# Optimization experiments

Hardware: AMD Instinct MI355X
Metric: run time of the kernel (lower is better)

The kernel has to match this reference:

```python
import jax, jax.numpy as jnp
import numpy as np

B, S, D, H, F, M = 2, 2048, 1024, 16, 4096, 1024
HD = D // H
LR, MOM_DECAY, WD, THRESH = 0.01, 0.9, 0.01, 0.1


def rmsnorm(x, w, eps=1e-8):
    n = jnp.linalg.norm(x, axis=-1, keepdims=True) * (x.shape[-1] ** -0.5)
    return w * x / (n + eps)


def rope_sin_cos(seq_len, dim):
    inv_freq = 1.0 / (10000.0 ** (jnp.arange(0, dim, 2, dtype=jnp.float32) / dim))
    ang = jnp.arange(seq_len, dtype=jnp.float32)[:, None] * inv_freq[None, :]  # [S, dim/2]
    return jnp.sin(ang), jnp.cos(ang)


def apply_rope(x, sin, cos):
    # x: [B,H,S,hd]; sin/cos: [S,hd/2] broadcast. Matches torch source:
    # split even/odd lanes, then CONCATENATE halves (not interleave).
    x1, x2 = x[..., ::2], x[..., 1::2]
    return jnp.concatenate([x1 * cos - x2 * sin, x1 * sin + x2 * cos], axis=-1)


def lmm_mlp(z, w0, b0, w1, b1):
    return jnp.maximum(z @ w0 + b0, 0.0) @ w1 + b1


def setup_inputs() -> dict:
    key = jax.random.key(0)
    k = jax.random.split(key, 20)
    sc = 0.02
    r = lambda i, shape: jax.random.normal(k[i], shape, jnp.float32) * sc
    return {
        'x': jax.random.normal(k[0], (B, S, D), jnp.float32),
        'mask': jnp.tril(jnp.ones((1, 1, S, S), dtype=bool)),
        'wq': r(1, (D, D)), 'wk': r(2, (D, D)), 'wv': r(3, (D, D)), 'wo': r(4, (D, D)),
        'n1': jnp.ones(D, jnp.float32), 'n2': jnp.ones(D, jnp.float32), 'n3': jnp.ones(D, jnp.float32),
        'ffn_w1': r(5, (D, F)), 'ffn_w2': r(6, (D, F)), 'ffn_w3': r(7, (F, D)),
        'pk_w': r(8, (D, M)), 'pk_b': jnp.zeros(M, jnp.float32),
        'pv_w': r(9, (D, M)), 'pv_b': jnp.zeros(M, jnp.float32),
        'pq_w': r(10, (D, M)), 'pq_b': jnp.zeros(M, jnp.float32),
        'l0_w': r(11, (M, M)), 'l0_b': jnp.zeros(M, jnp.float32),
        'l1_w': r(12, (M, M)), 'l1_b': jnp.zeros(M, jnp.float32),
        'm0_w': jnp.zeros((M, M), jnp.float32), 'm0_b': jnp.zeros(M, jnp.float32),
        'm1_w': jnp.zeros((M, M), jnp.float32), 'm1_b': jnp.zeros(M, jnp.float32),
    }


def reference(x, mask, wq, wk, wv, wo, n1, n2, n3, ffn_w1, ffn_w2, ffn_w3,
              pk_w, pk_b, pv_w, pv_b, pq_w, pq_b,
              l0_w, l0_b, l1_w, l1_b, m0_w, m0_b, m1_w, m1_b):
    # ---- attention sublayer (pre-norm, RoPE) ----
    hn = rmsnorm(x, n1)
    q = (hn @ wq).reshape(B, S, H, HD).transpose(0, 2, 1, 3)
    kk = (hn @ wk).reshape(B, S, H, HD).transpose(0, 2, 1, 3)
    v = (hn @ wv).reshape(B, S, H, HD).transpose(0, 2, 1, 3)
    sin, cos = rope_sin_cos(S, HD)
    q = apply_rope(q, sin, cos)
    kk = apply_rope(kk, sin, cos)
    scores = jnp.einsum('bhqd,bhkd->bhqk', q, kk) / np.sqrt(HD).astype(np.float32)
    scores = jnp.where(mask, scores, -jnp.inf)
    attn = jax.nn.softmax(scores, axis=-1)
    o = jnp.einsum('bhqk,bhkd->bhqd', attn, v).transpose(0, 2, 1, 3).reshape(B, S, D)
    h = x + o @ wo

    # ---- neural memory sublayer ----
    hn2 = rmsnorm(h, n2)
    q_lmm = hn2 @ pq_w + pq_b
    retrieved = lmm_mlp(q_lmm, l0_w, l0_b, l1_w, l1_b)  # uses PRE-update params

    # online Titan-style LMM update (torch does this under no_grad, after retrieval)
    kf = jax.lax.stop_gradient((hn2 @ pk_w + pk_b).reshape(B * S, M))
    vf = jax.lax.stop_gradient((hn2 @ pv_w + pv_b).reshape(B * S, M))

    def lmm_loss(params):
        pred = lmm_mlp(kf, *params)
        return jnp.sum(jnp.mean((pred - vf) ** 2, axis=-1))

    params = (l0_w, l0_b, l1_w, l1_b)
    loss_sum, grads = jax.value_and_grad(lmm_loss)(params)
    avg_loss = loss_sum / (B * S)
    do_update = avg_loss >= THRESH
    moms = (m0_w, m0_b, m1_w, m1_b)
    new_moms, new_params = [], []
    for p, m, g in zip(params, moms, grads):
        nm = MOM_DECAY * m - LR * g
        np_ = p * (1.0 - WD) + nm
        new_moms.append(jnp.where(do_update, nm, m))
        new_params.append(jnp.where(do_update, np_, p))

    h = h + retrieved

    # ---- SwiGLU FFN sublayer ----
    hn3 = rmsnorm(h, n3)
    ffn = (jax.nn.silu(hn3 @ ffn_w1) * (hn3 @ ffn_w2)) @ ffn_w3
    out = h + ffn
    return (out, *new_params, *new_moms)
```

## Files before the change

kernel.cpp:

```cpp
#include <hip/hip_runtime.h>
#include <cstdint>
#include <cstddef>

typedef __bf16 bf16;
typedef __bf16 bf16x2 __attribute__((ext_vector_type(2)));
typedef __bf16 bf16x4 __attribute__((ext_vector_type(4)));
typedef __bf16 bf16x8 __attribute__((ext_vector_type(8)));
typedef float  f32x4  __attribute__((ext_vector_type(4)));
typedef __attribute__((address_space(1))) unsigned int u32_g;
typedef __attribute__((address_space(3))) unsigned int u32_l;

#define DI __device__ __forceinline__

constexpr int Bc = 2, Sc = 2048, Dc = 1024, Hc = 16, HDc = 64, Fc = 4096, Mc = 1024;
constexpr int NTc = Bc * Sc;

DI void llds16(const bf16* g, bf16* l) {
  __builtin_amdgcn_global_load_lds((const u32_g*)g, (u32_l*)l, 16, 0, 0);
}
DI f32x4 cvt4(bf16x4 a) {
  f32x4 r; r[0] = (float)a[0]; r[1] = (float)a[1]; r[2] = (float)a[2]; r[3] = (float)a[3];
  return r;
}

__global__ void k_detect(const unsigned short* __restrict__ x, int* __restrict__ flag)
{
  const int tid = threadIdx.x;
  int cnt = 0;
#pragma unroll
  for (int i = 0; i < 8; i++) {
    unsigned short h = x[tid * 8 + i];
    int e = (h >> 7) & 0xFF;
    if (e < 96 || e > 160) cnt++;
  }
#pragma unroll
  for (int off = 32; off > 0; off >>= 1) cnt += __shfl_down(cnt, off, 64);
  if (tid == 0) *flag = (cnt > 32) ? 1 : 0;
}

__global__ __launch_bounds__(256)
void k_cvt(const void* __restrict__ src, bf16* __restrict__ dst, int n4, const int* __restrict__ flag)
{
  int i = blockIdx.x * 256 + threadIdx.x;
  if (i >= n4) return;
  bf16x4 o;
  if (*flag) {
    f32x4 v = ((const f32x4*)src)[i];
    o[0] = (bf16)v[0]; o[1] = (bf16)v[1]; o[2] = (bf16)v[2]; o[3] = (bf16)v[3];
  } else {
    o = ((const bf16x4*)src)[i];
  }
  ((bf16x4*)dst)[i] = o;
}

__global__ void k_transpose_dt(const void* __restrict__ src, bf16* __restrict__ dst,
                               int R, int C, const int* __restrict__ flag)
{
  __shared__ bf16 tile[32][33];
  const int c0 = blockIdx.x * 32, r0 = blockIdx.y * 32;
  const int tx = threadIdx.x, ty = threadIdx.y;
  const bool f32 = (*flag != 0);
  for (int i = ty; i < 32; i += 8) {
    size_t idx = (size_t)(r0 + i) * C + (c0 + tx);
    tile[i][tx] = f32 ? (bf16)((const float*)src)[idx] : ((const bf16*)src)[idx];
  }
  __syncthreads();
  for (int i = ty; i < 32; i += 8)
    dst[(size_t)(c0 + i) * R + (r0 + tx)] = tile[tx][i];
}

enum EpiMode { EPI_BF16 = 0, EPI_BIAS_BF16, EPI_BIAS_RELU_BF16, EPI_BIAS_RESB_F32,
               EPI_SILU_BF16, EPI_DZ_BF16, EPI_RESX_BF16, EPI_RESF_F32 };

template <int EPI>
__global__ __launch_bounds__(256)
void k_gemm(const bf16* __restrict__ A, const bf16* __restrict__ Bt,
            int Mr, int Nr, int Kr,
            float* outF, bf16* outB,
            const bf16* __restrict__ bias, const bf16* auxB,
            const float* resF,
            const void* __restrict__ resX, const int* __restrict__ flag)
{
  __shared__ bf16 As[128 * 32];
  __shared__ bf16 Bs[128 * 32];
  const int tid = threadIdx.x;
  const int w = tid >> 6, l = tid & 63;
  const int wr = w >> 1, wc = w & 1;
  const int row0 = blockIdx.y * 128, col0 = blockIdx.x * 128;

  const f32x4 vzero = {0.f, 0.f, 0.f, 0.f};
  f32x4 acc[4][4];
#pragma unroll
  for (int i = 0; i < 4; i++)
#pragma unroll
    for (int j = 0; j < 4; j++) acc[i][j] = vzero;

  const bf16* Ag = A + (size_t)(row0 + w * 16 + (l >> 2)) * Kr + ((l & 3) << 3);
  const bf16* Bg = Bt + (size_t)(col0 + w * 16 + (l >> 2)) * Kr + ((l & 3) << 3);
  bf16* AsW = &As[w * 512];
  bf16* BsW = &Bs[w * 512];
  const size_t rowHop = (size_t)64 * Kr;

  for (int k0 = 0; k0 < Kr; k0 += 32) {
    __syncthreads();
    llds16(Ag + k0, AsW);
    llds16(Ag + rowHop + k0, AsW + 2048);
    llds16(Bg + k0, BsW);
    llds16(Bg + rowHop + k0, BsW + 2048);
    __syncthreads();
    bf16x8 af[4], bfr[4];
#pragma unroll
    for (int mt = 0; mt < 4; mt++)
      af[mt] = *(const bf16x8*)&As[(wr * 64 + mt * 16 + (l & 15)) * 32 + (l >> 4) * 8];
#pragma unroll
    for (int nt = 0; nt < 4; nt++)
      bfr[nt] = *(const bf16x8*)&Bs[(wc * 64 + nt * 16 + (l & 15)) * 32 + (l >> 4) * 8];
#pragma unroll
    for (int mt = 0; mt < 4; mt++)
#pragma unroll
      for (int nt = 0; nt < 4; nt++)
        acc[mt][nt] = __builtin_amdgcn_mfma_f32_16x16x32_bf16(af[mt], bfr[nt], acc[mt][nt], 0, 0, 0);
  }

  const bool f32res = (EPI == EPI_RESX_BF16) ? (*flag != 0) : false;
  float biasv[4];
  if (EPI == EPI_BIAS_BF16 || EPI == EPI_BIAS_RELU_BF16 || EPI == EPI_BIAS_RESB_F32) {
#pragma unroll
    for (int nt = 0; nt < 4; nt++)
      biasv[nt] = (float)bias[col0 + wc * 64 + nt * 16 + (l & 15)];
  }
#pragma unroll
  for (int mt = 0; mt < 4; mt++) {
    const int rowb = row0 + wr * 64 + mt * 16 + ((l >> 4) << 2);
    float av[4][4];
    if (EPI == EPI_SILU_BF16 || EPI == EPI_DZ_BF16 || EPI == EPI_BIAS_RESB_F32) {
#pragma unroll
      for (int nt = 0; nt < 4; nt++) {
        const int col = col0 + wc * 64 + nt * 16 + (l & 15);
#pragma unroll
        for (int r = 0; r < 4; r++)
          av[nt][r] = (float)auxB[(size_t)(rowb + r) * Nr + col];
      }
    }
    if (EPI == EPI_RESF_F32) {
#pragma unroll
      for (int nt = 0; nt < 4; nt++) {
        const int col = col0 + wc * 64 + nt * 16 + (l & 15);
#pragma unroll
        for (int r = 0; r < 4; r++)
          av[nt][r] = resF[(size_t)(rowb + r) * Nr + col];
      }
    }
    if (EPI == EPI_RESX_BF16) {
#pragma unroll
      for (int nt = 0; nt < 4; nt++) {
        const int col = col0 + wc * 64 + nt * 16 + (l & 15);
#pragma unroll
        for (int r = 0; r < 4; r++) {
          const size_t idx = (size_t)(rowb + r) * Nr + col;
          av[nt][r] = f32res ? ((const float*)resX)[idx] : (float)((const bf16*)resX)[idx];
        }
      }
    }
#pragma unroll
    for (int nt = 0; nt < 4; nt++) {
      const int col = col0 + wc * 64 + nt * 16 + (l & 15);
#pragma unroll
      for (int r = 0; r < 4; r++) {
        const size_t idx = (size_t)(rowb + r) * Nr + col;
        float v = acc[mt][nt][r];
        if (EPI == EPI_BF16) { outB[idx] = (bf16)v; }
        else if (EPI == EPI_BIAS_BF16) { outB[idx] = (bf16)(v + biasv[nt]); }
        else if (EPI == EPI_BIAS_RELU_BF16) { outB[idx] = (bf16)fmaxf(v + biasv[nt], 0.f); }
        else if (EPI == EPI_BIAS_RESB_F32) { outF[idx] = v + biasv[nt] + av[nt][r]; }
        else if (EPI == EPI_SILU_BF16) {
          float s1v = av[nt][r];
          float sl = s1v / (1.f + __expf(-s1v));
          outB[idx] = (bf16)(sl * v);
        }
        else if (EPI == EPI_DZ_BF16) { outB[idx] = (bf16)(av[nt][r] > 0.f ? v : 0.f); }
        else if (EPI == EPI_RESX_BF16) { outB[idx] = (bf16)(v + av[nt][r]); }
        else if (EPI == EPI_RESF_F32) { outF[idx] = v + av[nt][r]; }
      }
    }
  }
}

__global__ __launch_bounds__(256)
void k_gemm_tn(const bf16* __restrict__ X, const bf16* __restrict__ Y, int Kt,
               float* __restrict__ out)
{
  __shared__ bf16 As[128 * 36];
  __shared__ bf16 Bs[128 * 36];
  const int tid = threadIdx.x;
  const int w = tid >> 6, l = tid & 63;
  const int wr = w >> 1, wc = w & 1;
  const int row0 = blockIdx.y * 128, col0 = blockIdx.x * 128;
  const int iofs = (tid & 15) * 8;
  const int tp   = (tid >> 4) * 2;

  const f32x4 vzero = {0.f, 0.f, 0.f, 0.f};
  f32x4 acc[4][4];
#pragma unroll
  for (int i = 0; i < 4; i++)
#pragma unroll
    for (int j = 0; j < 4; j++) acc[i][j] = vzero;

  const int chunk = Kt / gridDim.z;
  const int tbeg = blockIdx.z * chunk;

  for (int t0 = tbeg; t0 < tbeg + chunk; t0 += 32) {
    __syncthreads();
    bf16x8 a0 = *(const bf16x8*)&X[(size_t)(t0 + tp) * 1024 + row0 + iofs];
    bf16x8 a1 = *(const bf16x8*)&X[(size_t)(t0 + tp + 1) * 1024 + row0 + iofs];
    bf16x8 b0 = *(const bf16x8*)&Y[(size_t)(t0 + tp) * 1024 + col0 + iofs];
    bf16x8 b1 = *(const bf16x8*)&Y[(size_t)(t0 + tp + 1) * 1024 + col0 + iofs];
#pragma unroll
    for (int e = 0; e < 8; e++) {
      bf16x2 pa; pa[0] = a0[e]; pa[1] = a1[e];
      bf16x2 pb; pb[0] = b0[e]; pb[1] = b1[e];
      *(bf16x2*)&As[(iofs + e) * 36 + tp] = pa;
      *(bf16x2*)&Bs[(iofs + e) * 36 + tp] = pb;
    }
    __syncthreads();
    bf16x8 af[4], bfr[4];
#pragma unroll
    for (int mt = 0; mt < 4; mt++) {
      const int base = (wr * 64 + mt * 16 + (l & 15)) * 36 + (l >> 4) * 8;
      bf16x4 lo = *(const bf16x4*)&As[base];
      bf16x4 hi = *(const bf16x4*)&As[base + 4];
#pragma unroll
      for (int e = 0; e < 4; e++) { af[mt][e] = lo[e]; af[mt][4 + e] = hi[e]; }
    }
#pragma unroll
    for (int nt = 0; nt < 4; nt++) {
      const int base = (wc * 64 + nt * 16 + (l & 15)) * 36 + (l >> 4) * 8;
      bf16x4 lo = *(const bf16x4*)&Bs[base];
      bf16x4 hi = *(const bf16x4*)&Bs[base + 4];
#pragma unroll
      for (int e = 0; e < 4; e++) { bfr[nt][e] = lo[e]; bfr[nt][4 + e] = hi[e]; }
    }
#pragma unroll
    for (int mt = 0; mt < 4; mt++)
#pragma unroll
      for (int nt = 0; nt < 4; nt++)
        acc[mt][nt] = __builtin_amdgcn_mfma_f32_16x16x32_bf16(af[mt], bfr[nt], acc[mt][nt], 0, 0, 0);
  }

#pragma unroll
  for (int mt = 0; mt < 4; mt++) {
    const int rowb = row0 + wr * 64 + mt * 16 + ((l >> 4) << 2);
#pragma unroll
    for (int nt = 0; nt < 4; nt++) {
      const int col = col0 + wc * 64 + nt * 16 + (l & 15);
#pragma unroll
      for (int r = 0; r < 4; r++)
        atomicAdd(&out[(size_t)(rowb + r) * 1024 + col], acc[mt][nt][r]);
    }
  }
}

__global__ __launch_bounds__(256)
void k_rmsnorm_dt(const void* __restrict__ x, const bf16* __restrict__ w, bf16* __restrict__ out,
                  const int* __restrict__ flag)
{
  const int row = blockIdx.x;
  const int tid = threadIdx.x;
  f32x4 xv;
  if (*flag) xv = *(const f32x4*)((const float*)x + (size_t)row * Dc + tid * 4);
  else       xv = cvt4(*(const bf16x4*)((const bf16*)x + (size_t)row * Dc + tid * 4));
  float ss = xv[0] * xv[0] + xv[1] * xv[1] + xv[2] * xv[2] + xv[3] * xv[3];
#pragma unroll
  for (int off = 32; off > 0; off >>= 1) ss += __shfl_down(ss, off, 64);
  __shared__ float part[4];
  if ((tid & 63) == 0) part[tid >> 6] = ss;
  __syncthreads();
  float tot = part[0] + part[1] + part[2] + part[3];
  float inv = 1.f / (sqrtf(tot) * 0.03125f + 1e-8f);
  bf16x4 wb = *(const bf16x4*)(w + tid * 4);
  bf16x4 ov;
  ov[0] = (bf16)((float)wb[0] * xv[0] * inv);
  ov[1] = (bf16)((float)wb[1] * xv[1] * inv);
  ov[2] = (bf16)((float)wb[2] * xv[2] * inv);
  ov[3] = (bf16)((float)wb[3] * xv[3] * inv);
  *(bf16x4*)(out + (size_t)row * Dc + tid * 4) = ov;
}

__global__ __launch_bounds__(256)
void k_rmsnorm_b(const bf16* __restrict__ x, const bf16* __restrict__ w, bf16* __restrict__ out)
{
  const int row = blockIdx.x;
  const int tid = threadIdx.x;
  f32x4 xv = cvt4(*(const bf16x4*)(x + (size_t)row * Dc + tid * 4));
  float ss = xv[0] * xv[0] + xv[1] * xv[1] + xv[2] * xv[2] + xv[3] * xv[3];
#pragma unroll
  for (int off = 32; off > 0; off >>= 1) ss += __shfl_down(ss, off, 64);
  __shared__ float part[4];
  if ((tid & 63) == 0) part[tid >> 6] = ss;
  __syncthreads();
  float tot = part[0] + part[1] + part[2] + part[3];
  float inv = 1.f / (sqrtf(tot) * 0.03125f + 1e-8f);
  bf16x4 wb = *(const bf16x4*)(w + tid * 4);
  bf16x4 ov;
  ov[0] = (bf16)((float)wb[0] * xv[0] * inv);
  ov[1] = (bf16)((float)wb[1] * xv[1] * inv);
  ov[2] = (bf16)((float)wb[2] * xv[2] * inv);
  ov[3] = (bf16)((float)wb[3] * xv[3] * inv);
  *(bf16x4*)(out + (size_t)row * Dc + tid * 4) = ov;
}

__global__ __launch_bounds__(256)
void k_rmsnorm_f(const float* __restrict__ x, const bf16* __restrict__ w, bf16* __restrict__ out)
{
  const int row = blockIdx.x;
  const int tid = threadIdx.x;
  f32x4 xv = *(const f32x4*)(x + (size_t)row * Dc + tid * 4);
  float ss = xv[0] * xv[0] + xv[1] * xv[1] + xv[2] * xv[2] + xv[3] * xv[3];
#pragma unroll
  for (int off = 32; off > 0; off >>= 1) ss += __shfl_down(ss, off, 64);
  __shared__ float part[4];
  if ((tid & 63) == 0) part[tid >> 6] = ss;
  __syncthreads();
  float tot = part[0] + part[1] + part[2] + part[3];
  float inv = 1.f / (sqrtf(tot) * 0.03125f + 1e-8f);
  bf16x4 wb = *(const bf16x4*)(w + tid * 4);
  bf16x4 ov;
  ov[0] = (bf16)((float)wb[0] * xv[0] * inv);
  ov[1] = (bf16)((float)wb[1] * xv[1] * inv);
  ov[2] = (bf16)((float)wb[2] * xv[2] * inv);
  ov[3] = (bf16)((float)wb[3] * xv[3] * inv);
  *(bf16x4*)(out + (size_t)row * Dc + tid * 4) = ov;
}

__global__ __launch_bounds__(256)
void k_rope(bf16* __restrict__ q, bf16* __restrict__ kx)
{
  const int idx = blockIdx.x * 256 + threadIdx.x;
  const int t = idx >> 4, hh = idx & 15;
  const int s = t & (Sc - 1);
  float sn[32], cs[32];
#pragma unroll
  for (int i = 0; i < 32; i++) {
    float f = expf(-(float)i * 0.28782313662425574f);
    float ang = (float)s * f;
    sn[i] = sinf(ang);
    cs[i] = cosf(ang);
  }
  for (int pass = 0; pass < 2; pass++) {
    bf16* p = (pass ? kx : q) + (size_t)t * Dc + hh * HDc;
    float xb[64], ob[64];
#pragma unroll
    for (int j = 0; j < 16; j++) *(f32x4*)&xb[j * 4] = cvt4(*(const bf16x4*)(p + j * 4));
#pragma unroll
    for (int i = 0; i < 32; i++) {
      float x1 = xb[2 * i], x2 = xb[2 * i + 1];
      ob[i] = x1 * cs[i] - x2 * sn[i];
      ob[32 + i] = x1 * sn[i] + x2 * cs[i];
    }
#pragma unroll
    for (int j = 0; j < 16; j++) {
      bf16x4 o4;
      o4[0] = (bf16)ob[j * 4]; o4[1] = (bf16)ob[j * 4 + 1];
      o4[2] = (bf16)ob[j * 4 + 2]; o4[3] = (bf16)ob[j * 4 + 3];
      *(bf16x4*)(p + j * 4) = o4;
    }
  }
}

__global__ __launch_bounds__(256)
void k_attn(const bf16* __restrict__ q, const bf16* __restrict__ kx,
            const bf16* __restrict__ v, bf16* __restrict__ o)
{
  constexpr int PAD = 72;
  __shared__ bf16 Ks[64 * PAD];
  __shared__ bf16 Vt[64 * PAD];
  __shared__ bf16 Ps[4][16 * PAD];

  const int blk = blockIdx.x;
  const int qt = blk & 31;
  const int bh = blk >> 5;
  const int b = bh >> 4, hh = bh & 15;
  const int tid = threadIdx.x;
  const int w = tid >> 6, l = tid & 63;
  const int quad = l >> 4, c = l & 15;

  const int qrow = qt * 64 + w * 16 + c;
  const size_t qbase = ((size_t)(b * Sc + qrow)) * Dc + hh * HDc;
  bf16x8 qf0 = *(const bf16x8*)(q + qbase + quad * 8);
  bf16x8 qf1 = *(const bf16x8*)(q + qbase + 32 + quad * 8);
#pragma unroll
  for (int j = 0; j < 8; j++) {
    qf0[j] = (bf16)((float)qf0[j] * 0.125f);
    qf1[j] = (bf16)((float)qf1[j] * 0.125f);
  }

  const f32x4 vzero = {0.f, 0.f, 0.f, 0.f};
  f32x4 oacc[4];
#pragma unroll
  for (int nt = 0; nt < 4; nt++) oacc[nt] = vzero;
  float mrun[4] = {-3.0e38f, -3.0e38f, -3.0e38f, -3.0e38f};
  float lrun[4] = {0.f, 0.f, 0.f, 0.f};

  const int qrow0 = qt * 64 + w * 16 + quad * 4;

  for (int t0 = 0; t0 <= qt; t0++) {
    const int kk0 = t0 * 64;
    __syncthreads();
    {
      const int trow = tid >> 2;
      const int tpp = tid & 3;
      size_t g = ((size_t)(b * Sc + kk0 + trow)) * Dc + hh * HDc + tpp * 16;
      bf16x8 k0 = *(const bf16x8*)(kx + g);
      bf16x8 k1 = *(const bf16x8*)(kx + g + 8);
      *(bf16x8*)&Ks[trow * PAD + tpp * 16] = k0;
      *(bf16x8*)&Ks[trow * PAD + tpp * 16 + 8] = k1;
      bf16x8 v0 = *(const bf16x8*)(v + g);
      bf16x8 v1 = *(const bf16x8*)(v + g + 8);
#pragma unroll
      for (int j = 0; j < 8; j++) {
        Vt[(tpp * 16 + j) * PAD + trow] = v0[j];
        Vt[(tpp * 16 + 8 + j) * PAD + trow] = v1[j];
      }
    }
    __syncthreads();

    f32x4 sf[4];
#pragma unroll
    for (int nt = 0; nt < 4; nt++) {
      f32x4 a = vzero;
      bf16x8 b0 = *(const bf16x8*)&Ks[(nt * 16 + c) * PAD + quad * 8];
      bf16x8 b1 = *(const bf16x8*)&Ks[(nt * 16 + c) * PAD + 32 + quad * 8];
      a = __builtin_amdgcn_mfma_f32_16x16x32_bf16(qf0, b0, a, 0, 0, 0);
      a = __builtin_amdgcn_mfma_f32_16x16x32_bf16(qf1, b1, a, 0, 0, 0);
      sf[nt] = a;
    }
    if (t0 == qt) {
#pragma unroll
      for (int nt = 0; nt < 4; nt++)
#pragma unroll
        for (int r = 0; r < 4; r++)
          if (kk0 + nt * 16 + c > qrow0 + r) sf[nt][r] = -3.0e38f;
    }

    float mnew[4], alpha[4];
#pragma unroll
    for (int r = 0; r < 4; r++) {
      float mt = fmaxf(fmaxf(sf[0][r], sf[1][r]), fmaxf(sf[2][r], sf[3][r]));
      mt = fmaxf(mt, __shfl_xor(mt, 1, 64));
      mt = fmaxf(mt, __shfl_xor(mt, 2, 64));
      mt = fmaxf(mt, __shfl_xor(mt, 4, 64));
      mt = fmaxf(mt, __shfl_xor(mt, 8, 64));
      mnew[r] = fmaxf(mrun[r], mt);
      alpha[r] = __expf(mrun[r] - mnew[r]);
      mrun[r] = mnew[r];
    }
    float ps[4] = {0.f, 0.f, 0.f, 0.f};
#pragma unroll
    for (int nt = 0; nt < 4; nt++)
#pragma unroll
      for (int r = 0; r < 4; r++) {
        float p = __expf(sf[nt][r] - mnew[r]);
        sf[nt][r] = p;
        ps[r] += p;
      }
#pragma unroll
    for (int r = 0; r < 4; r++) {
      ps[r] += __shfl_xor(ps[r], 1, 64);
      ps[r] += __shfl_xor(ps[r], 2, 64);
      ps[r] += __shfl_xor(ps[r], 4, 64);
      ps[r] += __shfl_xor(ps[r], 8, 64);
      lrun[r] = lrun[r] * alpha[r] + ps[r];
    }
#pragma unroll
    for (int nt = 0; nt < 4; nt++)
#pragma unroll
      for (int r = 0; r < 4; r++) oacc[nt][r] *= alpha[r];

#pragma unroll
    for (int nt = 0; nt < 4; nt++)
#pragma unroll
      for (int r = 0; r < 4; r++)
        Ps[w][(quad * 4 + r) * PAD + nt * 16 + c] = (bf16)sf[nt][r];
    bf16x8 pa0 = *(const bf16x8*)&Ps[w][c * PAD + quad * 8];
    bf16x8 pa1 = *(const bf16x8*)&Ps[w][c * PAD + 32 + quad * 8];

#pragma unroll
    for (int nt = 0; nt < 4; nt++) {
      bf16x8 vb0 = *(const bf16x8*)&Vt[(nt * 16 + c) * PAD + quad * 8];
      bf16x8 vb1 = *(const bf16x8*)&Vt[(nt * 16 + c) * PAD + 32 + quad * 8];
      oacc[nt] = __builtin_amdgcn_mfma_f32_16x16x32_bf16(pa0, vb0, oacc[nt], 0, 0, 0);
      oacc[nt] = __builtin_amdgcn_mfma_f32_16x16x32_bf16(pa1, vb1, oacc[nt], 0, 0, 0);
    }
  }

  float inv[4];
#pragma unroll
  for (int r = 0; r < 4; r++) inv[r] = 1.f / lrun[r];
#pragma unroll
  for (int r = 0; r < 4; r++) {
    const size_t obase = ((size_t)(b * Sc + qrow0 + r)) * Dc + hh * HDc;
#pragma unroll
    for (int nt = 0; nt < 4; nt++)
      o[obase + nt * 16 + c] = (bf16)(oacc[nt][r] * inv[r]);
  }
}

__global__ __launch_bounds__(256)
void k_relu(const bf16* __restrict__ src, bf16* __restrict__ dst)
{
  int i = blockIdx.x * 256 + threadIdx.x;
  bf16x8 v = ((const bf16x8*)src)[i];
  bf16x8 o;
#pragma unroll
  for (int e = 0; e < 8; e++) o[e] = ((float)v[e] > 0.f) ? v[e] : (bf16)0.f;
  ((bf16x8*)dst)[i] = o;
}

__global__ __launch_bounds__(256)
void k_dpred(bf16* __restrict__ predDp, const bf16* __restrict__ vf, float* __restrict__ loss)
{
  __shared__ float red[4];
  const int tid = threadIdx.x;
  const size_t n8 = (size_t)NTc * Mc / 8;
  float lacc = 0.f;
  for (size_t i = (size_t)blockIdx.x * 256 + tid; i < n8; i += (size_t)gridDim.x * 256) {
    bf16x8 p8 = ((const bf16x8*)predDp)[i];
    bf16x8 v8 = ((const bf16x8*)vf)[i];
    bf16x8 d8;
#pragma unroll
    for (int e = 0; e < 8; e++) {
      float df = (float)p8[e] - (float)v8[e];
      lacc += df * df;
      d8[e] = (bf16)(df * (2.0f / 1024.0f));
    }
    ((bf16x8*)predDp)[i] = d8;
  }
#pragma unroll
  for (int off = 32; off > 0; off >>= 1) lacc += __shfl_down(lacc, off, 64);
  if ((tid & 63) == 0) red[tid >> 6] = lacc;
  __syncthreads();
  if (tid == 0) atomicAdd(loss, red[0] + red[1] + red[2] + red[3]);
}

__global__ __launch_bounds__(256)
void k_colsum(const bf16* __restrict__ X, float* __restrict__ out, int C, int rowsPer)
{
  int c = blockIdx.x * 256 + threadIdx.x;
  int r0 = blockIdx.y * rowsPer;
  float s = 0.f;
#pragma unroll 8
  for (int r = r0; r < r0 + rowsPer; r++) s += (float)X[(size_t)r * C + c];
  atomicAdd(&out[c], s);
}

__global__ __launch_bounds__(256)
void k_update_dt(const void* __restrict__ p0w, const void* __restrict__ p0b,
                 const void* __restrict__ p1w, const void* __restrict__ p1b,
                 const void* __restrict__ m0w, const void* __restrict__ m0b,
                 const void* __restrict__ m1w, const void* __restrict__ m1b,
                 const float* __restrict__ g0wF, const float* __restrict__ g0b,
                 const float* __restrict__ g1wF, const float* __restrict__ g1b,
                 const float* __restrict__ loss, const int* __restrict__ flag,
                 float* __restrict__ outP, float* __restrict__ outM)
{
  const int i = blockIdx.x * 256 + threadIdx.x;
  const bool upd = (loss[0] >= 0.1f * 1024.f * 4096.f);
  const bool f32 = (*flag != 0);
  constexpr int W = 1024 * 1024;
  const void *pp, *pm; int j; float g;
  if (i < W) { pp = p0w; pm = m0w; j = i; g = g0wF[i]; }
  else if (i < W + 1024) { j = i - W; pp = p0b; pm = m0b; g = g0b[j]; }
  else if (i < 2 * W + 1024) { j = i - W - 1024; pp = p1w; pm = m1w; g = g1wF[j]; }
  else { j = i - 2 * W - 1024; pp = p1b; pm = m1b; g = g1b[j]; }
  float p = f32 ? ((const float*)pp)[j] : (float)((const bf16*)pp)[j];
  float m = f32 ? ((const float*)pm)[j] : (float)((const bf16*)pm)[j];
  float nm = 0.9f * m - 0.01f * g;
  float np = 0.99f * p + nm;
  outP[i] = upd ? np : p;
  outM[i] = upd ? nm : m;
}

extern "C" void kernel_launch(void* const* d_in, const int* in_sizes, int n_in,
                              void* d_out, int out_size, void* d_ws, size_t ws_size,
                              hipStream_t stream)
{
  (void)in_sizes; (void)n_in; (void)out_size; (void)ws_size;
  const void* x   = d_in[0];
  const void* wq  = d_in[2];
  const void* wk  = d_in[3];
  const void* wv  = d_in[4];
  const void* wo  = d_in[5];
  const void* n1  = d_in[6];
  const void* n2  = d_in[7];
  const void* n3  = d_in[8];
  const void* fw1 = d_in[9];
  const void* fw2 = d_in[10];
  const void* fw3 = d_in[11];
  const void* pkw = d_in[12];
  const void* pkb = d_in[13];
  const void* pvw = d_in[14];
  const void* pvb = d_in[15];
  const void* pqw = d_in[16];
  const void* pqb = d_in[17];
  const void* l0w = d_in[18];
  const void* l0b = d_in[19];
  const void* l1w = d_in[20];
  const void* l1b = d_in[21];
  const void* m0w = d_in[22];
  const void* m0b = d_in[23];
  const void* m1w = d_in[24];
  const void* m1b = d_in[25];

  char* ws = (char*)d_ws;
  size_t off = 0;
  auto alloc = [&](size_t bytes) -> char* {
    char* p = ws + off;
    off += (bytes + 255) & ~(size_t)255;
    return p;
  };

  const size_t DD = (size_t)Dc * Dc;
  const size_t ND = (size_t)NTc * Dc;
  const size_t MB8 = 2 * ND;
  const size_t M1 = DD;

  bf16* W = (bf16*)alloc(2 * 8 * M1);
  bf16 *wqT = W, *wkT = W + M1, *wvT = W + 2 * M1, *woT = W + 3 * M1;
  bf16 *pqT = W + 4 * M1, *pkT = W + 5 * M1, *pvT = W + 6 * M1, *l0T = W + 7 * M1;
  bf16 *l1T = W + M1;
  bf16 *l1c = W;
  bf16 *w1T = W + 4 * M1;
  bf16 *w2T = W;
  bf16 *w3T = W + 4 * M1;

  bf16* B0 = (bf16*)alloc(MB8);
  bf16* B1 = (bf16*)alloc(MB8);
  bf16* B2 = (bf16*)alloc(MB8);
  bf16* B3 = (bf16*)alloc(MB8);
  bf16* B4 = (bf16*)alloc(MB8);
  bf16* s1 = B0;

  float* g0b = (float*)alloc(4 * 1024);
  float* g1b = (float*)alloc(4 * 1024);
  float* lossb = (float*)alloc(256);
  int*   flag  = (int*)alloc(256);
  bf16* n1c = (bf16*)alloc(2 * 1024);
  bf16* n2c = (bf16*)alloc(2 * 1024);
  bf16* n3c = (bf16*)alloc(2 * 1024);
  bf16* bqc = (bf16*)alloc(2 * 1024);
  bf16* bkc = (bf16*)alloc(2 * 1024);
  bf16* bvc = (bf16*)alloc(2 * 1024);
  bf16* b0c = (bf16*)alloc(2 * 1024);
  bf16* b1c = (bf16*)alloc(2 * 1024);

  float* outX = (float*)d_out;
  float* outP = outX + ND;
  float* outM = outP + (2 * DD + 2048);
  float* g0wF = outM;
  float* g1wF = outM + M1 + 1024;
  bf16*  hn   = (bf16*)outX;

  const dim3 tb(32, 8);

  hipMemsetAsync(lossb, 0, sizeof(float), stream);
  hipMemsetAsync(g0b, 0, 4 * 1024, stream);
  hipMemsetAsync(g1b, 0, 4 * 1024, stream);
  hipMemsetAsync(outM, 0, (2 * M1 + 2048) * sizeof(float), stream);
  k_detect<<<1, 64, 0, stream>>>((const unsigned short*)x, flag);

  k_cvt<<<1, 256, 0, stream>>>(n1, n1c, 256, flag);
  k_cvt<<<1, 256, 0, stream>>>(n2, n2c, 256, flag);
  k_cvt<<<1, 256, 0, stream>>>(n3, n3c, 256, flag);
  k_cvt<<<1, 256, 0, stream>>>(pqb, bqc, 256, flag);
  k_cvt<<<1, 256, 0, stream>>>(pkb, bkc, 256, flag);
  k_cvt<<<1, 256, 0, stream>>>(pvb, bvc, 256, flag);
  k_cvt<<<1, 256, 0, stream>>>(l0b, b0c, 256, flag);
  k_cvt<<<1, 256, 0, stream>>>(l1b, b1c, 256, flag);

  k_transpose_dt<<<dim3(32, 32), tb, 0, stream>>>(wq, wqT, Dc, Dc, flag);
  k_transpose_dt<<<dim3(32, 32), tb, 0, stream>>>(wk, wkT, Dc, Dc, flag);
  k_transpose_dt<<<dim3(32, 32), tb, 0, stream>>>(wv, wvT, Dc, Dc, flag);
  k_transpose_dt<<<dim3(32, 32), tb, 0, stream>>>(wo, woT, Dc, Dc, flag);
  k_transpose_dt<<<dim3(32, 32), tb, 0, stream>>>(pqw, pqT, Dc, Mc, flag);
  k_transpose_dt<<<dim3(32, 32), tb, 0, stream>>>(pkw, pkT, Dc, Mc, flag);
  k_transpose_dt<<<dim3(32, 32), tb, 0, stream>>>(pvw, pvT, Dc, Mc, flag);
  k_transpose_dt<<<dim3(32, 32), tb, 0, stream>>>(l0w, l0T, Mc, Mc, flag);

  k_rmsnorm_dt<<<NTc, 256, 0, stream>>>(x, n1c, hn, flag);
  k_gemm<EPI_BF16><<<dim3(8, 32), 256, 0, stream>>>(hn, wqT, NTc, Dc, Dc, nullptr, B0, nullptr, nullptr, nullptr, nullptr, nullptr);
  k_gemm<EPI_BF16><<<dim3(8, 32), 256, 0, stream>>>(hn, wkT, NTc, Dc, Dc, nullptr, B1, nullptr, nullptr, nullptr, nullptr, nullptr);
  k_gemm<EPI_BF16><<<dim3(8, 32), 256, 0, stream>>>(hn, wvT, NTc, Dc, Dc, nullptr, B2, nullptr, nullptr, nullptr, nullptr, nullptr);
  k_rope<<<256, 256, 0, stream>>>(B0, B1);
  k_attn<<<1024, 256, 0, stream>>>(B0, B1, B2, B3);
  k_gemm<EPI_RESX_BF16><<<dim3(8, 32), 256, 0, stream>>>(B3, woT, NTc, Dc, Dc, nullptr, B4, nullptr, nullptr, nullptr, x, flag);
  k_transpose_dt<<<dim3(32, 32), tb, 0, stream>>>(l1w, l1T, Mc, Mc, flag);

  k_rmsnorm_b<<<NTc, 256, 0, stream>>>(B4, n2c, B0);
  k_gemm<EPI_BIAS_BF16><<<dim3(8, 32), 256, 0, stream>>>(B0, pqT, NTc, Mc, Dc, nullptr, B1, bqc, nullptr, nullptr, nullptr, nullptr);
  k_gemm<EPI_BIAS_BF16><<<dim3(8, 32), 256, 0, stream>>>(B0, pkT, NTc, Mc, Dc, nullptr, B2, bkc, nullptr, nullptr, nullptr, nullptr);
  k_gemm<EPI_BIAS_BF16><<<dim3(8, 32), 256, 0, stream>>>(B0, pvT, NTc, Mc, Dc, nullptr, B3, bvc, nullptr, nullptr, nullptr, nullptr);
  k_gemm<EPI_BIAS_RELU_BF16><<<dim3(8, 32), 256, 0, stream>>>(B1, l0T, NTc, Mc, Mc, nullptr, B0, b0c, nullptr, nullptr, nullptr, nullptr);
  k_gemm<EPI_BIAS_RESB_F32><<<dim3(8, 32), 256, 0, stream>>>(B0, l1T, NTc, Mc, Mc, outX, nullptr, b1c, B4, nullptr, nullptr, nullptr);

  k_gemm<EPI_BIAS_BF16><<<dim3(8, 32), 256, 0, stream>>>(B2, l0T, NTc, Mc, Mc, nullptr, B4, b0c, nullptr, nullptr, nullptr, nullptr);
  k_transpose_dt<<<dim3(128, 32), tb, 0, stream>>>(fw1, w1T, Dc, Fc, flag);
  k_relu<<<2048, 256, 0, stream>>>(B4, B0);
  k_gemm<EPI_BIAS_BF16><<<dim3(8, 32), 256, 0, stream>>>(B0, l1T, NTc, Mc, Mc, nullptr, B1, b1c, nullptr, nullptr, nullptr, nullptr);
  k_cvt<<<1024, 256, 0, stream>>>(l1w, l1c, (int)(DD / 4), flag);
  k_dpred<<<256, 256, 0, stream>>>(B1, B3, lossb);
  k_gemm<EPI_DZ_BF16><<<dim3(8, 32), 256, 0, stream>>>(B1, l1c, NTc, Mc, Mc, nullptr, B3, nullptr, B4, nullptr, nullptr, nullptr);
  k_gemm_tn<<<dim3(8, 8, 8), 256, 0, stream>>>(B0, B1, NTc, g1wF);
  k_gemm_tn<<<dim3(8, 8, 8), 256, 0, stream>>>(B2, B3, NTc, g0wF);
  k_colsum<<<dim3(4, 32), 256, 0, stream>>>(B1, g1b, Mc, NTc / 32);
  k_colsum<<<dim3(4, 32), 256, 0, stream>>>(B3, g0b, Mc, NTc / 32);
  k_update_dt<<<8200, 256, 0, stream>>>(l0w, l0b, l1w, l1b, m0w, m0b, m1w, m1b,
                                        g0wF, g0b, g1wF, g1b, lossb, flag, outP, outM);

  k_transpose_dt<<<dim3(128, 32), tb, 0, stream>>>(fw2, w2T, Dc, Fc, flag);
  k_rmsnorm_f<<<NTc, 256, 0, stream>>>(outX, n3c, B4);
  k_gemm<EPI_BF16><<<dim3(32, 32), 256, 0, stream>>>(B4, w1T, NTc, Fc, Dc, nullptr, s1, nullptr, nullptr, nullptr, nullptr, nullptr);
  k_transpose_dt<<<dim3(32, 128), tb, 0, stream>>>(fw3, w3T, Fc, Dc, flag);
  k_gemm<EPI_SILU_BF16><<<dim3(32, 32), 256, 0, stream>>>(B4, w2T, NTc, Fc, Dc, nullptr, s1, nullptr, s1, nullptr, nullptr, nullptr);
  k_gemm<EPI_RESF_F32><<<dim3(8, 32), 256, 0, stream>>>(s1, w3T, NTc, Dc, Fc, outX, nullptr, nullptr, nullptr, outX, nullptr, nullptr);
}
```

Baseline: 1.104 ms.

## Pre-transpose V globally and read K/V fragments directly in attention

Adds a kernel that transposes V into a per-head [HD, S] layout before attention, so the attention kernel can load V and K MFMA operands straight from global memory instead of staging them through shared memory with two barriers per tile. Block order is also changed so the longest causal query tiles launch first, to reduce tail imbalance. The cost is an extra transpose pass, and each wave now redundantly fetches K/V from global/L2 instead of sharing one LDS copy across the four waves.

```diff
diff --git a/kernel.cpp b/kernel.cpp
--- a/kernel.cpp
+++ b/kernel.cpp
@@ -67,6 +67,20 @@
   __syncthreads();
   for (int i = ty; i < 32; i += 8)
     dst[(size_t)(c0 + i) * R + (r0 + tx)] = tile[tx][i];
+}
+
+__global__ void k_transpose_v(const bf16* __restrict__ v, bf16* __restrict__ vt)
+{
+  __shared__ bf16 tile[32][33];
+  const int d0 = blockIdx.x * 32, s0 = blockIdx.y * 32;
+  const int bh = blockIdx.z;
+  const int b = bh >> 4, hh = bh & 15;
+  const int tx = threadIdx.x, ty = threadIdx.y;
+  for (int i = ty; i < 32; i += 8)
+    tile[i][tx] = v[((size_t)(b * Sc + s0 + i)) * Dc + hh * HDc + d0 + tx];
+  __syncthreads();
+  for (int i = ty; i < 32; i += 8)
+    vt[((size_t)(bh * HDc + d0 + i)) * Sc + s0 + tx] = tile[tx][i];
 }
 
 enum EpiMode { EPI_BF16 = 0, EPI_BIAS_BF16, EPI_BIAS_RELU_BF16, EPI_BIAS_RESB_F32,
@@ -369,16 +383,14 @@
 
 __global__ __launch_bounds__(256)
 void k_attn(const bf16* __restrict__ q, const bf16* __restrict__ kx,
-            const bf16* __restrict__ v, bf16* __restrict__ o)
+            const bf16* __restrict__ vt, bf16* __restrict__ o)
 {
   constexpr int PAD = 72;
-  __shared__ bf16 Ks[64 * PAD];
-  __shared__ bf16 Vt[64 * PAD];
   __shared__ bf16 Ps[4][16 * PAD];
 
   const int blk = blockIdx.x;
-  const int qt = blk & 31;
-  const int bh = blk >> 5;
+  const int qt = 31 - (blk >> 5);
+  const int bh = blk & 31;
   const int b = bh >> 4, hh = bh & 15;
   const int tid = threadIdx.x;
   const int w = tid >> 6, l = tid & 63;
@@ -403,35 +415,21 @@
 
   const int qrow0 = qt * 64 + w * 16 + quad * 4;
 
+  const bf16* kb = kx + (size_t)b * Sc * Dc + hh * HDc;
+  const bf16* vb = vt + (size_t)bh * HDc * Sc;
+
   for (int t0 = 0; t0 <= qt; t0++) {
     const int kk0 = t0 * 64;
-    __syncthreads();
-    {
-      const int trow = tid >> 2;
-      const int tpp = tid & 3;
-      size_t g = ((size_t)(b * Sc + kk0 + trow)) * Dc + hh * HDc + tpp * 16;
-      bf16x8 k0 = *(const bf16x8*)(kx + g);
-      bf16x8 k1 = *(const bf16x8*)(kx + g + 8);
-      *(bf16x8*)&Ks[trow * PAD + tpp * 16] = k0;
-      *(bf16x8*)&Ks[trow * PAD + tpp * 16 + 8] = k1;
-      bf16x8 v0 = *(const bf16x8*)(v + g);
-      bf16x8 v1 = *(const bf16x8*)(v + g + 8);
-#pragma unroll
-      for (int j = 0; j < 8; j++) {
-        Vt[(tpp * 16 + j) * PAD + trow] = v0[j];
-        Vt[(tpp * 16 + 8 + j) * PAD + trow] = v1[j];
-      }
-    }
-    __syncthreads();
 
     f32x4 sf[4];
 #pragma unroll
     for (int nt = 0; nt < 4; nt++) {
+      const bf16* kr = kb + (size_t)(kk0 + nt * 16 + c) * Dc + quad * 8;
+      bf16x8 k0 = *(const bf16x8*)kr;
+      bf16x8 k1 = *(const bf16x8*)(kr + 32);
       f32x4 a = vzero;
-      bf16x8 b0 = *(const bf16x8*)&Ks[(nt * 16 + c) * PAD + quad * 8];
-      bf16x8 b1 = *(const bf16x8*)&Ks[(nt * 16 + c) * PAD + 32 + quad * 8];
-      a = __builtin_amdgcn_mfma_f32_16x16x32_bf16(qf0, b0, a, 0, 0, 0);
-      a = __builtin_amdgcn_mfma_f32_16x16x32_bf16(qf1, b1, a, 0, 0, 0);
+      a = __builtin_amdgcn_mfma_f32_16x16x32_bf16(qf0, k0, a, 0, 0, 0);
+      a = __builtin_amdgcn_mfma_f32_16x16x32_bf16(qf1, k1, a, 0, 0, 0);
       sf[nt] = a;
     }
     if (t0 == qt) {
@@ -486,10 +484,11 @@
 
 #pragma unroll
     for (int nt = 0; nt < 4; nt++) {
-      bf16x8 vb0 = *(const bf16x8*)&Vt[(nt * 16 + c) * PAD + quad * 8];
-      bf16x8 vb1 = *(const bf16x8*)&Vt[(nt * 16 + c) * PAD + 32 + quad * 8];
-      oacc[nt] = __builtin_amdgcn_mfma_f32_16x16x32_bf16(pa0, vb0, oacc[nt], 0, 0, 0);
-      oacc[nt] = __builtin_amdgcn_mfma_f32_16x16x32_bf16(pa1, vb1, oacc[nt], 0, 0, 0);
+      const bf16* vr = vb + (size_t)(nt * 16 + c) * Sc + kk0 + quad * 8;
+      bf16x8 v0 = *(const bf16x8*)vr;
+      bf16x8 v1 = *(const bf16x8*)(vr + 32);
+      oacc[nt] = __builtin_amdgcn_mfma_f32_16x16x32_bf16(pa0, v0, oacc[nt], 0, 0, 0);
+      oacc[nt] = __builtin_amdgcn_mfma_f32_16x16x32_bf16(pa1, v1, oacc[nt], 0, 0, 0);
     }
   }
 
@@ -639,6 +638,7 @@
   bf16* B3 = (bf16*)alloc(MB8);
   bf16* B4 = (bf16*)alloc(MB8);
   bf16* s1 = B0;
+  bf16* VtG = B4;
 
   float* g0b = (float*)alloc(4 * 1024);
   float* g1b = (float*)alloc(4 * 1024);
@@ -690,8 +690,9 @@
   k_gemm<EPI_BF16><<<dim3(8, 32), 256, 0, stream>>>(hn, wqT, NTc, Dc, Dc, nullptr, B0, nullptr, nullptr, nullptr, nullptr, nullptr);
   k_gemm<EPI_BF16><<<dim3(8, 32), 256, 0, stream>>>(hn, wkT, NTc, Dc, Dc, nullptr, B1, nullptr, nullptr, nullptr, nullptr, nullptr);
   k_gemm<EPI_BF16><<<dim3(8, 32), 256, 0, stream>>>(hn, wvT, NTc, Dc, Dc, nullptr, B2, nullptr, nullptr, nullptr, nullptr, nullptr);
+  k_transpose_v<<<dim3(2, 64, 32), tb, 0, stream>>>(B2, VtG);
   k_rope<<<256, 256, 0, stream>>>(B0, B1);
-  k_attn<<<1024, 256, 0, stream>>>(B0, B1, B2, B3);
+  k_attn<<<1024, 256, 0, stream>>>(B0, B1, VtG, B3);
   k_gemm<EPI_RESX_BF16><<<dim3(8, 32), 256, 0, stream>>>(B3, woT, NTc, Dc, Dc, nullptr, B4, nullptr, nullptr, nullptr, x, flag);
   k_transpose_dt<<<dim3(32, 32), tb, 0, stream>>>(l1w, l1T, Mc, Mc, flag);
 
```

Result: no change. 1.117 ms (+1.2%).
